# Performance work log

Hardware: AMD Instinct MI355X
Metric: run time of the kernel (lower is better)

The kernel has to match this reference:

```python
import jax, jax.numpy as jnp
import numpy as np

N = 100000   # nodes
E = 1600000  # edges
F = 128      # node features
H = 64       # hidden_dim
G = 64       # graphs in batch


def setup_inputs() -> dict:
    key = jax.random.key(0)
    ks = jax.random.split(key, 12)
    x = jax.random.normal(ks[0], (N, F), jnp.float32)
    edge_index = jax.random.randint(ks[1], (2, E), 0, N, dtype=jnp.int64)
    batch = jnp.sort(jax.random.randint(ks[2], (N,), 0, G, dtype=jnp.int64))
    s = 0.05
    W1 = jax.random.normal(ks[3], (F, H), jnp.float32) * s
    b1 = jnp.zeros((H,), jnp.float32)
    W2 = jax.random.normal(ks[4], (H, H), jnp.float32) * s
    b2 = jnp.zeros((H,), jnp.float32)
    Wa = jax.random.normal(ks[5], (H, 1), jnp.float32) * s
    ba = jnp.zeros((1,), jnp.float32)
    Wc = jax.random.normal(ks[6], (H, 1), jnp.float32) * s
    bc = jnp.zeros((1,), jnp.float32)
    return {"x": x, "edge_index": edge_index, "batch": batch,
            "W1": W1, "b1": b1, "W2": W2, "b2": b2,
            "Wa": Wa, "ba": ba, "Wc": Wc, "bc": bc}


def _gcn_norm(edge_index, n):
    # Add self-loops, compute symmetric normalization deg^-1/2[src]*deg^-1/2[dst]
    loop = jnp.arange(n, dtype=edge_index.dtype)
    src = jnp.concatenate([edge_index[0], loop])
    dst = jnp.concatenate([edge_index[1], loop])
    deg = jax.ops.segment_sum(jnp.ones_like(src, jnp.float32), dst, num_segments=n)
    dinv = jnp.where(deg > 0, deg ** -0.5, 0.0)
    norm = dinv[src] * dinv[dst]  # [E+N]
    return src, dst, norm


def _gcn_conv(x, W, b, src, dst, norm, n):
    h = x @ W                         # [n, H] dense transform first (PyG order)
    msg = h[src] * norm[:, None]      # gather + normalize [E+n, H]
    agg = jax.ops.segment_sum(msg, dst, num_segments=n)  # scatter-add
    return agg + b


def reference(x, edge_index, batch, W1, b1, W2, b2, Wa, ba, Wc, bc):
    n = x.shape[0]
    src, dst, norm = _gcn_norm(edge_index, n)
    h = jax.nn.relu(_gcn_conv(x, W1, b1, src, dst, norm, n))
    # dropout p=0.1 is identity in eval mode
    h = jax.nn.relu(_gcn_conv(h, W2, b2, src, dst, norm, n))
    action_logits = (h @ Wa + ba)[:, 0]  # [N]
    counts = jax.ops.segment_sum(jnp.ones((n,), jnp.float32), batch, num_segments=G)
    pooled = jax.ops.segment_sum(h, batch, num_segments=G) / jnp.maximum(counts, 1.0)[:, None]
    value = pooled @ Wc + bc  # [G, 1]
    return action_logits, value
```

## Files before the change

kernel.cpp:

```cpp
#include <hip/hip_runtime.h>
#include <hip/hip_fp16.h>
#include <math.h>

#define FEAT 128
#define HID  64
#define BSH  7
#define BNODES (1 << BSH)
#define PB   256
#define SRCM ((1u << 25) - 1)
#define PSPLIT 16

typedef _Float16 f16_t;
typedef f16_t half8 __attribute__((ext_vector_type(8)));
typedef float  f32x4 __attribute__((ext_vector_type(4)));


__global__ void part_hist_k(const int* __restrict__ dst, int* __restrict__ table,
                            float* __restrict__ pooled, int e, int nb, int gh) {
    if (blockIdx.x == 0) {
        for (int i = threadIdx.x; i < gh; i += 256) pooled[i] = 0.0f;
    }
    __shared__ int lcnt[1024];
    for (int i = threadIdx.x; i < nb; i += 256) lcnt[i] = 0;
    __syncthreads();
    int eb = (e + PB - 1) / PB;
    int lo = blockIdx.x * eb, hi = min(lo + eb, e);
    for (int i = lo + threadIdx.x; i < hi; i += 256)
        atomicAdd(&lcnt[dst[i] >> BSH], 1);
    __syncthreads();
    for (int k = threadIdx.x; k < nb; k += 256)
        table[k * PB + blockIdx.x] = lcnt[k];
}

__global__ void scan1_k(int* __restrict__ data, int* __restrict__ aux, int L) {
    __shared__ int s[1024];
    int gid = blockIdx.x * 1024 + threadIdx.x;
    int v = (gid < L) ? data[gid] : 0;
    s[threadIdx.x] = v;
    __syncthreads();
    for (int off = 1; off < 1024; off <<= 1) {
        int t = (threadIdx.x >= off) ? s[threadIdx.x - off] : 0;
        __syncthreads();
        s[threadIdx.x] += t;
        __syncthreads();
    }
    if (gid < L) data[gid] = s[threadIdx.x] - v;
    if (threadIdx.x == 1023) aux[blockIdx.x] = s[1023];
}

__global__ void scan2_k(int* aux, int naux) {
    __shared__ int s[1024];
    int v = (threadIdx.x < naux) ? aux[threadIdx.x] : 0;
    s[threadIdx.x] = v;
    __syncthreads();
    for (int off = 1; off < 1024; off <<= 1) {
        int t = (threadIdx.x >= off) ? s[threadIdx.x - off] : 0;
        __syncthreads();
        s[threadIdx.x] += t;
        __syncthreads();
    }
    if (threadIdx.x < naux) aux[threadIdx.x] = s[threadIdx.x] - v;
}

__global__ void part_scatter_k(const int* __restrict__ src, const int* __restrict__ dst,
                               const int* __restrict__ table, const int* __restrict__ aux,
                               unsigned* __restrict__ packed, int e, int nb) {
    __shared__ int loff[1024];
    for (int k = threadIdx.x; k < nb; k += 256) {
        int idx = k * PB + blockIdx.x;
        loff[k] = table[idx] + aux[idx >> 10];
    }
    __syncthreads();
    int eb = (e + PB - 1) / PB;
    int lo = blockIdx.x * eb, hi = min(lo + eb, e);
    for (int i = lo + threadIdx.x; i < hi; i += 256) {
        int d = dst[i];
        int p = atomicAdd(&loff[d >> BSH], 1);
        packed[p] = ((unsigned)(d & (BNODES - 1)) << 25) | (unsigned)src[i];
    }
}


__global__ void bucket_sort_k(const unsigned* __restrict__ packed,
                              const int* __restrict__ table, const int* __restrict__ aux,
                              int* __restrict__ col, int* __restrict__ rowptr,
                              float* __restrict__ dinv, int n, int e, int nb) {
    __shared__ int cnt[BNODES];
    __shared__ int s[BNODES];
    __shared__ int cur[BNODES];
    const int k = blockIdx.x;
    const int t = threadIdx.x;
    if (t < BNODES) cnt[t] = 0;
    __syncthreads();
    int i0 = k * PB;
    int i1 = (k + 1) * PB;
    const int bs = table[i0] + aux[i0 >> 10];
    const int be = (k + 1 < nb) ? (table[i1] + aux[i1 >> 10]) : e;
    for (int i = bs + t; i < be; i += 256)
        atomicAdd(&cnt[packed[i] >> 25], 1);
    __syncthreads();
    if (t < BNODES) s[t] = cnt[t];
    __syncthreads();
    for (int off = 1; off < BNODES; off <<= 1) {
        int v = (t < BNODES && t >= off) ? s[t - off] : 0;
        __syncthreads();
        if (t < BNODES) s[t] += v;
        __syncthreads();
    }
    if (t < BNODES) {
        int base = bs + s[t] - cnt[t];
        cur[t] = base;
        int node = (k << BSH) + t;
        if (node < n) {
            rowptr[node] = base;
            dinv[node] = 1.0f / sqrtf(1.0f + (float)cnt[t]);
            if (node == n - 1) rowptr[n] = base + cnt[t];
        }
    }
    __syncthreads();
    for (int i = bs + t; i < be; i += 256) {
        unsigned u = packed[i];
        int p = atomicAdd(&cur[u >> 25], 1);
        col[p] = (int)(u & SRCM);
    }
}


__global__ __launch_bounds__(256, 3)
void gemm_tile_k(const float* __restrict__ X, const float* __restrict__ W,
                 const float* __restrict__ dinv, __half* __restrict__ out,
                 const float* __restrict__ W2, __half* __restrict__ w2h, int n) {
    constexpr int K = FEAT;
    __shared__ float sX[64][K + 4];
    __shared__ float sW[64][64];
    const int row0 = blockIdx.x * 64;
    const int t  = threadIdx.x;
    const int tx = t & 15;
    const int ty = t >> 4;

    if (blockIdx.x == 0) {
        for (int i = t; i < HID * HID; i += 256) {
            int c = i >> 6, k = i & 63;
            w2h[i] = __float2half(W2[k * HID + c]);
        }
    }

    const float* xb = X + (size_t)row0 * K;
#pragma unroll
    for (int it = 0; it < K / 16; ++it) {
        int fl = it * 1024 + t * 4;
        int r  = fl >> 7;
        int k  = fl & (K - 1);
        float4 v = make_float4(0.f, 0.f, 0.f, 0.f);
        if (row0 + r < n) v = *(const float4*)(xb + fl);
        *(float4*)&sX[r][k] = v;
    }

    float acc[4][4] = {};
#pragma unroll
    for (int ph = 0; ph < K / 64; ++ph) {
        __syncthreads();
#pragma unroll
        for (int it = 0; it < 4; ++it) {
            int fl = it * 1024 + t * 4;
            *(float4*)&sW[fl >> 6][fl & 63] = *(const float4*)(W + ph * 64 * HID + fl);
        }
        __syncthreads();

#pragma unroll 8
        for (int k = 0; k < 64; k += 4) {
            float4 a[4], b[4];
#pragma unroll
            for (int i = 0; i < 4; i++) a[i] = *(float4*)&sX[ty * 4 + i][ph * 64 + k];
#pragma unroll
            for (int j = 0; j < 4; j++) b[j] = *(float4*)&sW[k + j][tx * 4];
#pragma unroll
            for (int i = 0; i < 4; i++) {
                acc[i][0] = fmaf(a[i].x, b[0].x, acc[i][0]);
                acc[i][1] = fmaf(a[i].x, b[0].y, acc[i][1]);
                acc[i][2] = fmaf(a[i].x, b[0].z, acc[i][2]);
                acc[i][3] = fmaf(a[i].x, b[0].w, acc[i][3]);
                acc[i][0] = fmaf(a[i].y, b[1].x, acc[i][0]);
                acc[i][1] = fmaf(a[i].y, b[1].y, acc[i][1]);
                acc[i][2] = fmaf(a[i].y, b[1].z, acc[i][2]);
                acc[i][3] = fmaf(a[i].y, b[1].w, acc[i][3]);
                acc[i][0] = fmaf(a[i].z, b[2].x, acc[i][0]);
                acc[i][1] = fmaf(a[i].z, b[2].y, acc[i][1]);
                acc[i][2] = fmaf(a[i].z, b[2].z, acc[i][2]);
                acc[i][3] = fmaf(a[i].z, b[2].w, acc[i][3]);
                acc[i][0] = fmaf(a[i].w, b[3].x, acc[i][0]);
                acc[i][1] = fmaf(a[i].w, b[3].y, acc[i][1]);
                acc[i][2] = fmaf(a[i].w, b[3].z, acc[i][2]);
                acc[i][3] = fmaf(a[i].w, b[3].w, acc[i][3]);
            }
        }
    }

#pragma unroll
    for (int i = 0; i < 4; i++) {
        int gr = row0 + ty * 4 + i;
        if (gr < n) {
            float sc = dinv[gr];
            union { __half2 h[2]; unsigned long long u; } pk;
            pk.h[0] = __floats2half2_rn(acc[i][0] * sc, acc[i][1] * sc);
            pk.h[1] = __floats2half2_rn(acc[i][2] * sc, acc[i][3] * sc);
            *(unsigned long long*)(out + (size_t)gr * HID + tx * 4) = pk.u;
        }
    }
}


__global__ __launch_bounds__(512)
void gather1t2_k(const __half* __restrict__ tS, const int* __restrict__ rowptr,
                 const int* __restrict__ col, const float* __restrict__ dinv,
                 const float* __restrict__ b, const __half* __restrict__ w2h,
                 __half* __restrict__ out, int n) {
    __shared__ __half sh[16][72];
    const int tid  = threadIdx.x;
    const int nl   = tid >> 5;
    const int lane = tid & 31;
    const int r0   = blockIdx.x * 16;
    const int node = r0 + nl;

    float h0 = 0.f, h1 = 0.f;
    if (node < n) {
        int beg = rowptr[node], end = rowptr[node + 1];
        const __half2* tl = (const __half2*)tS + lane;
        float2 acc = __half22float2(tl[node * 32]);
        int e = beg;
        for (; e + 16 <= end; e += 16) {
            int s[16];
            __half2 v[16];
#pragma unroll
            for (int j = 0; j < 16; j++) s[j] = col[e + j];
#pragma unroll
            for (int j = 0; j < 16; j++) v[j] = tl[s[j] * 32];
            float2 t0 = make_float2(0.f, 0.f), t1 = make_float2(0.f, 0.f);
#pragma unroll
            for (int j = 0; j < 8; j++) {
                float2 f = __half22float2(v[j]);
                t0.x += f.x; t0.y += f.y;
            }
#pragma unroll
            for (int j = 8; j < 16; j++) {
                float2 f = __half22float2(v[j]);
                t1.x += f.x; t1.y += f.y;
            }
            acc.x += t0.x + t1.x;
            acc.y += t0.y + t1.y;
        }
        for (; e + 4 <= end; e += 4) {
            __half2 v0 = tl[col[e] * 32];
            __half2 v1 = tl[col[e + 1] * 32];
            __half2 v2 = tl[col[e + 2] * 32];
            __half2 v3 = tl[col[e + 3] * 32];
            float2 f0 = __half22float2(v0), f1 = __half22float2(v1);
            float2 f2 = __half22float2(v2), f3 = __half22float2(v3);
            acc.x += (f0.x + f1.x) + (f2.x + f3.x);
            acc.y += (f0.y + f1.y) + (f2.y + f3.y);
        }
        for (; e < end; ++e) {
            float2 f = __half22float2(tl[col[e] * 32]);
            acc.x += f.x; acc.y += f.y;
        }
        float d = dinv[node];
        float2 bb = *(const float2*)(b + 2 * lane);
        h0 = fmaxf(fmaf(d, acc.x, bb.x), 0.0f);
        h1 = fmaxf(fmaf(d, acc.y, bb.y), 0.0f);
    }
    *(__half2*)&sh[nl][2 * lane] = __floats2half2_rn(h0, h1);
    __syncthreads();

    const int w = tid >> 6;
    if (w < 4) {
        const int l    = tid & 63;
        const int colc = l & 15;
        const int kb   = l >> 4;
        const int t    = w;
        const __half* wp = w2h + (size_t)(t * 16 + colc) * HID + kb * 8;
        half8 b0 = *(const half8*)(wp);
        half8 b1 = *(const half8*)(wp + 32);
        half8 a0 = *(const half8*)&sh[colc][kb * 8];
        half8 a1 = *(const half8*)&sh[colc][32 + kb * 8];
        f32x4 acc = {};
        acc = __builtin_amdgcn_mfma_f32_16x16x32_f16(a0, b0, acc, 0, 0, 0);
        acc = __builtin_amdgcn_mfma_f32_16x16x32_f16(a1, b1, acc, 0, 0, 0);
        const int rbase = r0 + kb * 4;
#pragma unroll
        for (int r = 0; r < 4; ++r) {
            int gr = rbase + r;
            if (gr < n) {
                float dv = dinv[gr];
                out[(size_t)gr * HID + t * 16 + colc] = __float2half(acc[r] * dv);
            }
        }
    }
}


__global__ void gather2_k(const __half* __restrict__ tS, const int* __restrict__ rowptr,
                          const int* __restrict__ col, const float* __restrict__ dinv,
                          const float* __restrict__ b, __half* __restrict__ out,
                          const float* __restrict__ Wa, const float* __restrict__ ba,
                          float* __restrict__ logits, int n) {
    int node = (int)((blockIdx.x * (size_t)blockDim.x + threadIdx.x) >> 5);
    int lane = threadIdx.x & 31;
    if (node >= n) return;
    int beg = rowptr[node], end = rowptr[node + 1];
    const __half2* tl = (const __half2*)tS + lane;
    float2 acc = __half22float2(tl[node * 32]);
    int e = beg;
    for (; e + 16 <= end; e += 16) {
        int s[16];
        __half2 v[16];
#pragma unroll
        for (int j = 0; j < 16; j++) s[j] = col[e + j];
#pragma unroll
        for (int j = 0; j < 16; j++) v[j] = tl[s[j] * 32];
        float2 t0 = make_float2(0.f, 0.f), t1 = make_float2(0.f, 0.f);
#pragma unroll
        for (int j = 0; j < 8; j++) {
            float2 f = __half22float2(v[j]);
            t0.x += f.x; t0.y += f.y;
        }
#pragma unroll
        for (int j = 8; j < 16; j++) {
            float2 f = __half22float2(v[j]);
            t1.x += f.x; t1.y += f.y;
        }
        acc.x += t0.x + t1.x;
        acc.y += t0.y + t1.y;
    }
    for (; e + 4 <= end; e += 4) {
        __half2 v0 = tl[col[e] * 32];
        __half2 v1 = tl[col[e + 1] * 32];
        __half2 v2 = tl[col[e + 2] * 32];
        __half2 v3 = tl[col[e + 3] * 32];
        float2 f0 = __half22float2(v0), f1 = __half22float2(v1);
        float2 f2 = __half22float2(v2), f3 = __half22float2(v3);
        acc.x += (f0.x + f1.x) + (f2.x + f3.x);
        acc.y += (f0.y + f1.y) + (f2.y + f3.y);
    }
    for (; e < end; ++e) {
        float2 f = __half22float2(tl[col[e] * 32]);
        acc.x += f.x; acc.y += f.y;
    }
    float d = dinv[node];
    float2 bb = *(const float2*)(b + 2 * lane);
    float h0 = fmaxf(fmaf(d, acc.x, bb.x), 0.0f);
    float h1 = fmaxf(fmaf(d, acc.y, bb.y), 0.0f);
    ((__half2*)out)[node * 32 + lane] = __floats2half2_rn(h0, h1);
    float2 wa = *(const float2*)(Wa + 2 * lane);
    float p = h0 * wa.x + h1 * wa.y;
#pragma unroll
    for (int off = 16; off > 0; off >>= 1) p += __shfl_down(p, off, 32);
    if (lane == 0) logits[node] = p + ba[0];
}


__global__ void pool2_k(const __half* __restrict__ h, const int* __restrict__ batch,
                        float* __restrict__ pooled, int n) {
    const int gid  = blockIdx.x / PSPLIT;
    const int part = blockIdx.x % PSPLIT;
    int lo = 0, hi = n;
    while (lo < hi) { int m = (lo + hi) >> 1; if (batch[m] < gid) lo = m + 1; else hi = m; }
    const int b0 = lo;
    hi = n;
    while (lo < hi) { int m = (lo + hi) >> 1; if (batch[m] < gid + 1) lo = m + 1; else hi = m; }
    const int b1 = lo;
    const int chunk = (b1 - b0 + PSPLIT - 1) / PSPLIT;
    const int r0 = b0 + part * chunk;
    const int r1 = min(r0 + chunk, b1);
    const int lane = threadIdx.x & 31;
    const int rg   = threadIdx.x >> 5;
    const __half2* hp = (const __half2*)h + lane;
    float2 acc = make_float2(0.f, 0.f);
    for (int i = r0 + rg; i < r1; i += 8) {
        float2 f = __half22float2(hp[(size_t)i * 32]);
        acc.x += f.x; acc.y += f.y;
    }
    __shared__ float2 red[8][32];
    red[rg][lane] = acc;
    __syncthreads();
    if (threadIdx.x < 32) {
        float2 s = make_float2(0.f, 0.f);
#pragma unroll
        for (int r = 0; r < 8; r++) { s.x += red[r][threadIdx.x].x; s.y += red[r][threadIdx.x].y; }
        atomicAdd(&pooled[gid * HID + 2 * threadIdx.x], s.x);
        atomicAdd(&pooled[gid * HID + 2 * threadIdx.x + 1], s.y);
    }
}


__global__ void value_k(const float* __restrict__ pooled, const int* __restrict__ batch,
                        const float* __restrict__ Wc, const float* __restrict__ bc,
                        float* __restrict__ val, int n, int g) {
    int gw   = (int)((blockIdx.x * (size_t)blockDim.x + threadIdx.x) >> 6);
    int lane = threadIdx.x & 63;
    if (gw >= g) return;
    int lo = 0, hi = n;
    while (lo < hi) { int m = (lo + hi) >> 1; if (batch[m] < gw) lo = m + 1; else hi = m; }
    int b0 = lo;
    lo = 0; hi = n;
    while (lo < hi) { int m = (lo + hi) >> 1; if (batch[m] < gw + 1) lo = m + 1; else hi = m; }
    float cnt = fmaxf((float)(lo - b0), 1.0f);
    float p = (pooled[gw * HID + lane] / cnt) * Wc[lane];
#pragma unroll
    for (int off = 32; off > 0; off >>= 1) p += __shfl_down(p, off);
    if (lane == 0) val[gw] = p + bc[0];
}

extern "C" void kernel_launch(void* const* d_in, const int* in_sizes, int n_in,
                              void* d_out, int out_size, void* d_ws, size_t ws_size,
                              hipStream_t stream) {
    const float* x     = (const float*)d_in[0];
    const int*   ei    = (const int*)d_in[1];
    const int*   batch = (const int*)d_in[2];
    const float* W1    = (const float*)d_in[3];
    const float* b1    = (const float*)d_in[4];
    const float* W2    = (const float*)d_in[5];
    const float* b2    = (const float*)d_in[6];
    const float* Wa    = (const float*)d_in[7];
    const float* ba    = (const float*)d_in[8];
    const float* Wc    = (const float*)d_in[9];
    const float* bc    = (const float*)d_in[10];

    const int n = in_sizes[0] / FEAT;
    const int e = in_sizes[1] / 2;
    const int g = out_size - n;
    const int* src = ei;
    const int* dst = ei + e;

    const int nb = (n + BNODES - 1) >> BSH;
    const int L  = nb * PB;

    float*    ws     = (float*)d_ws;
    float*    dinv   = ws;
    float*    bufA   = dinv + n;
    float*    bufB   = bufA + (size_t)n * HID;
    float*    pooled = bufB + (size_t)n * HID;
    __half*   w2h    = (__half*)(pooled + (size_t)g * HID);
    int*      table  = (int*)(w2h + HID * HID);
    int*      aux    = table + L;
    int*      rowptr = aux + 1024;
    int*      col    = rowptr + n + 1;
    unsigned* packed = (unsigned*)bufA;
    __half*   tS1    = (__half*)bufA;
    __half*   tS2    = (__half*)bufB;
    __half*   h2     = (__half*)bufA;

    const int B = 256;
    const int gridT  = (n + 63) / 64;
    const int gridG  = (int)(((size_t)n * 32 + B - 1) / B);
    const int gridF  = (n + 15) / 16;
    const int nb1    = (L + 1023) / 1024;

    part_hist_k<<<PB, B, 0, stream>>>(dst, table, pooled, e, nb, g * HID);
    scan1_k<<<nb1, 1024, 0, stream>>>(table, aux, L);
    scan2_k<<<1, 1024, 0, stream>>>(aux, nb1);
    part_scatter_k<<<PB, B, 0, stream>>>(src, dst, table, aux, packed, e, nb);
    bucket_sort_k<<<nb, B, 0, stream>>>(packed, table, aux, col, rowptr, dinv, n, e, nb);

    gemm_tile_k<<<gridT, B, 0, stream>>>(x, W1, dinv, tS1, W2, w2h, n);
    gather1t2_k<<<gridF, 512, 0, stream>>>(tS1, rowptr, col, dinv, b1, w2h, tS2, n);

    gather2_k<<<gridG, B, 0, stream>>>(tS2, rowptr, col, dinv, b2, h2,
                                       Wa, ba, (float*)d_out, n);

    pool2_k<<<g * PSPLIT, B, 0, stream>>>(h2, batch, pooled, n);
    value_k<<<(g * 64 + B - 1) / B, B, 0, stream>>>(pooled, batch, Wc, bc,
                                                    (float*)d_out + n, n, g);
}
```

Measured before the change: 294.4 us.

## Replace fp32 tiled first-layer GEMM with fp16 MFMA kernel

```diff
diff --git a/kernel.cpp b/kernel.cpp
--- a/kernel.cpp
+++ b/kernel.cpp
@@ -84,12 +84,24 @@
 __global__ void bucket_sort_k(const unsigned* __restrict__ packed,
                               const int* __restrict__ table, const int* __restrict__ aux,
                               int* __restrict__ col, int* __restrict__ rowptr,
-                              float* __restrict__ dinv, int n, int e, int nb) {
+                              float* __restrict__ dinv, int n, int e, int nb,
+                              const float* __restrict__ W1, const float* __restrict__ W2,
+                              __half* __restrict__ w1h, __half* __restrict__ w2h) {
     __shared__ int cnt[BNODES];
     __shared__ int s[BNODES];
     __shared__ int cur[BNODES];
     const int k = blockIdx.x;
     const int t = threadIdx.x;
+    if (k == 0) {
+        for (int i = t; i < FEAT * HID; i += 256) {
+            int c = i >> 7, kk = i & 127;
+            w1h[i] = __float2half(W1[kk * HID + c]);
+        }
+        for (int i = t; i < HID * HID; i += 256) {
+            int c = i >> 6, kk = i & 63;
+            w2h[i] = __float2half(W2[kk * HID + c]);
+        }
+    }
     if (t < BNODES) cnt[t] = 0;
     __syncthreads();
     int i0 = k * PB;
@@ -126,85 +138,55 @@
 }
 
 
-__global__ __launch_bounds__(256, 3)
-void gemm_tile_k(const float* __restrict__ X, const float* __restrict__ W,
-                 const float* __restrict__ dinv, __half* __restrict__ out,
-                 const float* __restrict__ W2, __half* __restrict__ w2h, int n) {
-    constexpr int K = FEAT;
-    __shared__ float sX[64][K + 4];
-    __shared__ float sW[64][64];
-    const int row0 = blockIdx.x * 64;
-    const int t  = threadIdx.x;
-    const int tx = t & 15;
-    const int ty = t >> 4;
-
-    if (blockIdx.x == 0) {
-        for (int i = t; i < HID * HID; i += 256) {
-            int c = i >> 6, k = i & 63;
-            w2h[i] = __float2half(W2[k * HID + c]);
-        }
-    }
-
-    const float* xb = X + (size_t)row0 * K;
-#pragma unroll
-    for (int it = 0; it < K / 16; ++it) {
-        int fl = it * 1024 + t * 4;
-        int r  = fl >> 7;
-        int k  = fl & (K - 1);
-        float4 v = make_float4(0.f, 0.f, 0.f, 0.f);
-        if (row0 + r < n) v = *(const float4*)(xb + fl);
-        *(float4*)&sX[r][k] = v;
-    }
-
-    float acc[4][4] = {};
-#pragma unroll
-    for (int ph = 0; ph < K / 64; ++ph) {
-        __syncthreads();
-#pragma unroll
-        for (int it = 0; it < 4; ++it) {
-            int fl = it * 1024 + t * 4;
-            *(float4*)&sW[fl >> 6][fl & 63] = *(const float4*)(W + ph * 64 * HID + fl);
-        }
-        __syncthreads();
-
-#pragma unroll 8
-        for (int k = 0; k < 64; k += 4) {
-            float4 a[4], b[4];
-#pragma unroll
-            for (int i = 0; i < 4; i++) a[i] = *(float4*)&sX[ty * 4 + i][ph * 64 + k];
-#pragma unroll
-            for (int j = 0; j < 4; j++) b[j] = *(float4*)&sW[k + j][tx * 4];
-#pragma unroll
-            for (int i = 0; i < 4; i++) {
-                acc[i][0] = fmaf(a[i].x, b[0].x, acc[i][0]);
-                acc[i][1] = fmaf(a[i].x, b[0].y, acc[i][1]);
-                acc[i][2] = fmaf(a[i].x, b[0].z, acc[i][2]);
-                acc[i][3] = fmaf(a[i].x, b[0].w, acc[i][3]);
-                acc[i][0] = fmaf(a[i].y, b[1].x, acc[i][0]);
-                acc[i][1] = fmaf(a[i].y, b[1].y, acc[i][1]);
-                acc[i][2] = fmaf(a[i].y, b[1].z, acc[i][2]);
-                acc[i][3] = fmaf(a[i].y, b[1].w, acc[i][3]);
-                acc[i][0] = fmaf(a[i].z, b[2].x, acc[i][0]);
-                acc[i][1] = fmaf(a[i].z, b[2].y, acc[i][1]);
-                acc[i][2] = fmaf(a[i].z, b[2].z, acc[i][2]);
-                acc[i][3] = fmaf(a[i].z, b[2].w, acc[i][3]);
-                acc[i][0] = fmaf(a[i].w, b[3].x, acc[i][0]);
-                acc[i][1] = fmaf(a[i].w, b[3].y, acc[i][1]);
-                acc[i][2] = fmaf(a[i].w, b[3].z, acc[i][2]);
-                acc[i][3] = fmaf(a[i].w, b[3].w, acc[i][3]);
+__global__ __launch_bounds__(256)
+void gemm1_mfma_k(const float* __restrict__ X, const __half* __restrict__ w1h,
+                  const float* __restrict__ dinv, __half* __restrict__ out, int n) {
+    const int wave  = threadIdx.x >> 6;
+    const int l     = threadIdx.x & 63;
+    const int strip = blockIdx.x * 4 + wave;
+    const int r0    = strip * 16;
+    if (r0 >= n) return;
+    const int colc = l & 15;
+    const int kb   = l >> 4;
+    const int arow = r0 + colc;
+
+    half8 a[4];
+    {
+        const float* xp = X + (size_t)arow * FEAT + kb * 8;
+        const bool rok = arow < n;
+#pragma unroll
+        for (int q = 0; q < 4; ++q) {
+            float4 v0 = make_float4(0.f, 0.f, 0.f, 0.f), v1 = v0;
+            if (rok) {
+                v0 = *(const float4*)(xp + q * 32);
+                v1 = *(const float4*)(xp + q * 32 + 4);
             }
-        }
-    }
-
-#pragma unroll
-    for (int i = 0; i < 4; i++) {
-        int gr = row0 + ty * 4 + i;
-        if (gr < n) {
-            float sc = dinv[gr];
-            union { __half2 h[2]; unsigned long long u; } pk;
-            pk.h[0] = __floats2half2_rn(acc[i][0] * sc, acc[i][1] * sc);
-            pk.h[1] = __floats2half2_rn(acc[i][2] * sc, acc[i][3] * sc);
-            *(unsigned long long*)(out + (size_t)gr * HID + tx * 4) = pk.u;
+            half8 av;
+            av[0] = (f16_t)v0.x; av[1] = (f16_t)v0.y; av[2] = (f16_t)v0.z; av[3] = (f16_t)v0.w;
+            av[4] = (f16_t)v1.x; av[5] = (f16_t)v1.y; av[6] = (f16_t)v1.z; av[7] = (f16_t)v1.w;
+            a[q] = av;
+        }
+    }
+
+    const int rbase = r0 + kb * 4;
+    float dv[4];
+#pragma unroll
+    for (int r = 0; r < 4; ++r) dv[r] = (rbase + r < n) ? dinv[rbase + r] : 0.f;
+
+#pragma unroll
+    for (int t = 0; t < 4; ++t) {
+        const __half* wp = w1h + (size_t)(t * 16 + colc) * FEAT + kb * 8;
+        f32x4 acc = {};
+#pragma unroll
+        for (int q = 0; q < 4; ++q) {
+            half8 bq = *(const half8*)(wp + q * 32);
+            acc = __builtin_amdgcn_mfma_f32_16x16x32_f16(a[q], bq, acc, 0, 0, 0);
+        }
+#pragma unroll
+        for (int r = 0; r < 4; ++r) {
+            int gr = rbase + r;
+            if (gr < n)
+                out[(size_t)gr * HID + t * 16 + colc] = __float2half(acc[r] * dv[r]);
         }
     }
 }
@@ -290,8 +272,8 @@
         for (int r = 0; r < 4; ++r) {
             int gr = rbase + r;
             if (gr < n) {
-                float dv = dinv[gr];
-                out[(size_t)gr * HID + t * 16 + colc] = __float2half(acc[r] * dv);
+                float dvv = dinv[gr];
+                out[(size_t)gr * HID + t * 16 + colc] = __float2half(acc[r] * dvv);
             }
         }
     }
@@ -440,7 +422,8 @@
     float*    bufB   = bufA + (size_t)n * HID;
     float*    pooled = bufB + (size_t)n * HID;
     __half*   w2h    = (__half*)(pooled + (size_t)g * HID);
-    int*      table  = (int*)(w2h + HID * HID);
+    __half*   w1h    = w2h + HID * HID;
+    int*      table  = (int*)(w1h + FEAT * HID);
     int*      aux    = table + L;
     int*      rowptr = aux + 1024;
     int*      col    = rowptr + n + 1;
@@ -450,18 +433,20 @@
     __half*   h2     = (__half*)bufA;
 
     const int B = 256;
-    const int gridT  = (n + 63) / 64;
     const int gridG  = (int)(((size_t)n * 32 + B - 1) / B);
     const int gridF  = (n + 15) / 16;
+    const int strips = (n + 15) / 16;
+    const int gridM  = (strips + 3) / 4;
     const int nb1    = (L + 1023) / 1024;
 
     part_hist_k<<<PB, B, 0, stream>>>(dst, table, pooled, e, nb, g * HID);
     scan1_k<<<nb1, 1024, 0, stream>>>(table, aux, L);
     scan2_k<<<1, 1024, 0, stream>>>(aux, nb1);
     part_scatter_k<<<PB, B, 0, stream>>>(src, dst, table, aux, packed, e, nb);
-    bucket_sort_k<<<nb, B, 0, stream>>>(packed, table, aux, col, rowptr, dinv, n, e, nb);
-
-    gemm_tile_k<<<gridT, B, 0, stream>>>(x, W1, dinv, tS1, W2, w2h, n);
+    bucket_sort_k<<<nb, B, 0, stream>>>(packed, table, aux, col, rowptr, dinv, n, e, nb,
+                                        W1, W2, w1h, w2h);
+
+    gemm1_mfma_k<<<gridM, B, 0, stream>>>(x, w1h, dinv, tS1, n);
     gather1t2_k<<<gridF, 512, 0, stream>>>(tS1, rowptr, col, dinv, b1, w2h, tS2, n);
 
     gather2_k<<<gridG, B, 0, stream>>>(tS2, rowptr, col, dinv, b2, h2,
```

After: 295.3 us. No clear change (+0.3%).
